# Performance work log

Hardware: AMD Instinct MI355X
Metric: run time of the kernel (lower is better)

Reference implementation:

```python
import jax, jax.numpy as jnp
import numpy as np

NUM_HEADS = 4
ALPHA = 0.2  # LeakyReLU negative slope


def setup_inputs() -> dict:
    key = jax.random.key(0)
    k1, k2 = jax.random.split(key)
    input_tensor = jax.random.normal(k1, (2, 4096, 128), dtype=jnp.float32)
    adj_matrix = jax.random.randint(k2, (4096, 4096), 0, 2, dtype=jnp.int32)
    return {"input_tensor": input_tensor, "adj_matrix": adj_matrix}


def reference(input_tensor, adj_matrix):
    B, S, F = input_tensor.shape
    H = NUM_HEADS
    x = input_tensor.reshape(B, S, H, F // H)          # (B,S,H,K)
    # full dense score matrix, QK^T-like with shared projection (identity)
    scores = jnp.einsum('bihk,bjhk->bhij', x, x)        # (B,H,S,S)
    scores = jax.nn.leaky_relu(scores, negative_slope=ALPHA)
    # adjacency mask broadcast over (B,H)
    scores = jnp.where(adj_matrix[None, None, :, :] == 0, -jnp.inf, scores)
    probs = jax.nn.softmax(scores, axis=-1)             # dropout p=0 -> identity
    out = jnp.einsum('bhij,bjhk->bihk', probs, x)       # (B,S,H,K)
    return out.reshape(B, S, F)                          # concat=True
```

## Files before the change

### kernel.cpp

```cpp
#include <hip/hip_runtime.h>
#include <stdint.h>

#define SEQ 4096
#define FDIM 128
#define NH 4
#define HD 32
#define NB 2
#define NROWS (NB * NH * SEQ)
#define LOG2E 1.4426950408889634f
#define VCOL 68
#define VHALF (32 * VCOL)

typedef float f32x4 __attribute__((ext_vector_type(4)));
typedef __bf16 bf16x8 __attribute__((ext_vector_type(8)));

__device__ __forceinline__ unsigned short f2bf(float f) {
  unsigned int u = __builtin_bit_cast(unsigned int, f);
  return (unsigned short)((u + 0x7FFFu + ((u >> 16) & 1u)) >> 16);
}

__global__ void cvt_kernel(const float* __restrict__ in, unsigned short* __restrict__ out) {
  int i = (blockIdx.x * 256 + threadIdx.x) * 4;
  float4 v = *reinterpret_cast<const float4*>(in + i);
  ushort4 o;
  o.x = f2bf(v.x); o.y = f2bf(v.y); o.z = f2bf(v.z); o.w = f2bf(v.w);
  *reinterpret_cast<ushort4*>(out + i) = o;
}

__global__ void adjpack_kernel(const int* __restrict__ adj, unsigned short* __restrict__ bits16) {
  size_t t = (size_t)blockIdx.x * 256 + threadIdx.x;
  const uint4* p = reinterpret_cast<const uint4*>(adj) + t * 4;
  uint4 a = p[0], b = p[1], c = p[2], d = p[3];
  unsigned m = 0;
  m |= (a.x != 0) ? 1u : 0u;        m |= (a.y != 0) ? 2u : 0u;
  m |= (a.z != 0) ? 4u : 0u;        m |= (a.w != 0) ? 8u : 0u;
  m |= (b.x != 0) ? 16u : 0u;       m |= (b.y != 0) ? 32u : 0u;
  m |= (b.z != 0) ? 64u : 0u;       m |= (b.w != 0) ? 128u : 0u;
  m |= (c.x != 0) ? 256u : 0u;      m |= (c.y != 0) ? 512u : 0u;
  m |= (c.z != 0) ? 1024u : 0u;     m |= (c.w != 0) ? 2048u : 0u;
  m |= (d.x != 0) ? 4096u : 0u;     m |= (d.y != 0) ? 8192u : 0u;
  m |= (d.z != 0) ? 16384u : 0u;    m |= (d.w != 0) ? 32768u : 0u;
  bits16[t] = (unsigned short)m;
}

#define STEP(T, RB, WBUF)                                                       \
  {                                                                             \
    __syncthreads();                                                            \
    const bool pfok = (T) + 1 < NT;                                             \
    if (pfok) {      \
      kptr += 64 * FDIM;                                                        \
      kload = *reinterpret_cast<const uint4*>(kptr);                            \
      sptr += 64 * FDIM;                                                        \
      r0 = *reinterpret_cast<const uint2*>(sptr);                               \
      r1 = *reinterpret_cast<const uint2*>(sptr + FDIM);                        \
      wnext = brow[bcol0 + (T) + 1];                                            \
    }                                                                           \
    f32x4 sc[4];                                                                \
    __builtin_amdgcn_s_setprio(1);                                              \
    _Pragma("unroll") for (int t4 = 0; t4 < 4; ++t4) {                          \
      bf16x8 kf = __builtin_bit_cast(bf16x8,                                    \
          *reinterpret_cast<const uint4*>(&Kl[RB][t4 * 16 + ql][g * 8]));       \
      sc[t4] = __builtin_amdgcn_mfma_f32_16x16x32_bf16(kf, qf, zf, 0, 0, 0);    \
    }                                                                           \
    __builtin_amdgcn_s_setprio(0);                                              \
    const unsigned long long wsh = wcur >> (4 * g);                             \
    const unsigned mwl = (unsigned)wsh, mwh = (unsigned)(wsh >> 32);            \
    float pf4[4][4];                                                            \
    _Pragma("unroll") for (int t4 = 0; t4 < 4; ++t4) {                          \
      const unsigned word = (t4 & 2) ? mwh : mwl;                               \
      _Pragma("unroll") for (int r = 0; r < 4; ++r) {                           \
        float v = sc[t4][r];                                                    \
        v = fmaxf(v, 0.2f * v);                                 \
        float e = __builtin_amdgcn_exp2f(v);                \
        const int pos = 16 * (t4 & 1) + r;                                      \
        const unsigned msk = (unsigned)((int)(word << (31 - pos)) >> 31);       \
        pf4[t4][r] = __builtin_bit_cast(                                        \
            float, __builtin_bit_cast(unsigned, e) & msk);                      \
      }                                                                         \
    }                                                                           \
    __builtin_amdgcn_s_setprio(1);                                              \
    _Pragma("unroll") for (int u = 0; u < 2; ++u) {                             \
      bf16x8 pa;                                                                \
      _Pragma("unroll") for (int tp = 0; tp < 2; ++tp)                          \
          _Pragma("unroll") for (int r = 0; r < 4; ++r)                         \
              pa[tp * 4 + r] = (__bf16)pf4[2 * u + tp][r];                      \
      bf16x8 vf0 = __builtin_bit_cast(bf16x8,                                   \
          *reinterpret_cast<const uint4*>(&Vp[RB][ql * VCOL + u * 32 + g * 8]));        \
      bf16x8 vf1 = __builtin_bit_cast(bf16x8,                                   \
          *reinterpret_cast<const uint4*>(&Vp[RB][(16 + ql) * VCOL + u * 32 + g * 8])); \
      acc0 = __builtin_amdgcn_mfma_f32_16x16x32_bf16(pa, vf0, acc0, 0, 0, 0);   \
      acc1 = __builtin_amdgcn_mfma_f32_16x16x32_bf16(pa, vf1, acc1, 0, 0, 0);   \
      accL = __builtin_amdgcn_mfma_f32_16x16x32_bf16(pa, ones, accL, 0, 0, 0);  \
    }                                                                           \
    __builtin_amdgcn_s_setprio(0);                                              \
    if (pfok) {   \
      *reinterpret_cast<uint4*>(&Kl[WBUF][krow][kq * 8]) = kload;               \
      unsigned* vw = reinterpret_cast<unsigned*>(&Vp[WBUF][0]) + pi0h;          \
      vw[(4 * c4 + 0) * 34] = __builtin_amdgcn_perm(r1.x, r0.x, selA);          \
      vw[(4 * c4 + 1) * 34] = __builtin_amdgcn_perm(r1.x, r0.x, selB);          \
      vw[(4 * c4 + 2) * 34] = __builtin_amdgcn_perm(r1.y, r0.y, selA);          \
      vw[(4 * c4 + 3) * 34] = __builtin_amdgcn_perm(r1.y, r0.y, selB);          \
    }                                                                           \
    wcur = wnext;                                                               \
  }

template <int NSPLIT>
__global__ __launch_bounds__(256, 4) void gat_kernel(
    const unsigned short* __restrict__ xbf,
    const unsigned long long* __restrict__ bits,
    float* __restrict__ dst,
    float* __restrict__ lbuf) {
  __shared__ __align__(16) unsigned short Kl[2][64][40];
  __shared__ __align__(16) unsigned short Vp[2][VHALF];

  const int bh = blockIdx.y;
  const int b = bh >> 2;
  const int h = bh & 3;
  const int tid = threadIdx.x;
  const int wid = tid >> 6;
  const int lane = tid & 63;
  const int g = lane >> 4;
  const int ql = lane & 15;
  const int qw = blockIdx.x * 64 + wid * 16;
  const int jbase = blockIdx.z * (SEQ / NSPLIT);
  const int NT = (SEQ / NSPLIT) / 64;

  const unsigned short* xb = xbf + ((size_t)b * SEQ) * FDIM + h * HD;

  bf16x8 qraw = __builtin_bit_cast(bf16x8,
      *reinterpret_cast<const uint4*>(xb + (size_t)(qw + ql) * FDIM + g * 8));
  bf16x8 qf;
#pragma unroll
  for (int e = 0; e < 8; ++e) qf[e] = (__bf16)((float)qraw[e] * LOG2E);

  bf16x8 ones;
#pragma unroll
  for (int e = 0; e < 8; ++e) ones[e] = (__bf16)1.0f;
  const f32x4 zf = {0.f, 0.f, 0.f, 0.f};

  f32x4 acc0 = {0.f, 0.f, 0.f, 0.f};
  f32x4 acc1 = {0.f, 0.f, 0.f, 0.f};
  f32x4 accL = {0.f, 0.f, 0.f, 0.f};

  const unsigned long long* brow = bits + (size_t)(qw + ql) * (SEQ / 64);
  const int bcol0 = jbase >> 6;

  const int krow = tid >> 2;
  const int kq = tid & 3;
  const unsigned short* kptr = xb + (size_t)(jbase + krow) * FDIM + kq * 8;

  const int s3 = (tid >> 3) & 7;
  const int pr = (s3 & 1) | (((s3 >> 1) & 1) << 1) | ((wid & 1) << 2) |
                 (((s3 >> 2) & 1) << 3) | ((wid >> 1) << 4);
  const int c4 = tid & 7;
  const unsigned short* sptr = xb + (size_t)(jbase + 2 * pr) * FDIM + c4 * 4;

  const int pi0h = 16 * (pr >> 4) + 4 * ((pr >> 1) & 3) + 2 * ((pr >> 3) & 1) + (pr & 1);

  const unsigned selA = 0x05040100u;
  const unsigned selB = 0x07060302u;

  uint4 kload = *reinterpret_cast<const uint4*>(kptr);
  uint2 r0 = *reinterpret_cast<const uint2*>(sptr);
  uint2 r1 = *reinterpret_cast<const uint2*>(sptr + FDIM);
  unsigned long long wcur = brow[bcol0];
  unsigned long long wnext = 0;
  *reinterpret_cast<uint4*>(&Kl[0][krow][kq * 8]) = kload;
  {
    unsigned* vw = reinterpret_cast<unsigned*>(&Vp[0][0]) + pi0h;
    vw[(4 * c4 + 0) * 34] = __builtin_amdgcn_perm(r1.x, r0.x, selA);
    vw[(4 * c4 + 1) * 34] = __builtin_amdgcn_perm(r1.x, r0.x, selB);
    vw[(4 * c4 + 2) * 34] = __builtin_amdgcn_perm(r1.y, r0.y, selA);
    vw[(4 * c4 + 3) * 34] = __builtin_amdgcn_perm(r1.y, r0.y, selB);
  }

  for (int t = 0; t < NT; t += 2) {
    STEP(t, 0, 1);
    STEP(t + 1, 1, 0);
  }

  if (NSPLIT == 1) {
#pragma unroll
    for (int r = 0; r < 4; ++r) {
      const float inv = 1.f / accL[r];
      const size_t o = ((size_t)b * SEQ + (size_t)(qw + 4 * g + r)) * FDIM + h * HD;
      dst[o + ql] = acc0[r] * inv;
      dst[o + 16 + ql] = acc1[r] * inv;
    }
  } else {
    float* Op = dst + (((size_t)blockIdx.z * (NB * NH) + bh) * SEQ) * HD;
#pragma unroll
    for (int r = 0; r < 4; ++r) {
      const int q = qw + 4 * g + r;
      Op[(size_t)q * HD + ql] = acc0[r];
      Op[(size_t)q * HD + 16 + ql] = acc1[r];
    }
    if (ql == 0) {
#pragma unroll
      for (int r = 0; r < 4; ++r)
        lbuf[(size_t)blockIdx.z * NROWS + (size_t)bh * SEQ + qw + 4 * g + r] = accL[r];
    }
  }
}

template <int NSPLIT>
__global__ __launch_bounds__(256) void combine_kernel(
    const float* __restrict__ Op, const float* __restrict__ lbuf, float* __restrict__ out) {
  const int idx = blockIdx.x * 256 + threadIdx.x;
  const int row = idx >> 3;
  const int dc = (idx & 7) * 4;
  float lt = 0.f;
  float4 o = {0.f, 0.f, 0.f, 0.f};
#pragma unroll
  for (int s = 0; s < NSPLIT; ++s) {
    lt += lbuf[(size_t)s * NROWS + row];
    float4 v = *reinterpret_cast<const float4*>(Op + ((size_t)s * NROWS + row) * HD + dc);
    o.x += v.x; o.y += v.y; o.z += v.z; o.w += v.w;
  }
  const float inv = 1.f / lt;
  const int bh = row >> 12;
  const int q = row & (SEQ - 1);
  const int b = bh >> 2;
  const int h = bh & 3;
  float4 w;
  w.x = o.x * inv; w.y = o.y * inv; w.z = o.z * inv; w.w = o.w * inv;
  *reinterpret_cast<float4*>(out + ((size_t)b * SEQ + q) * FDIM + h * HD + dc) = w;
}

extern "C" void kernel_launch(void* const* d_in, const int* in_sizes, int n_in,
                              void* d_out, int out_size, void* d_ws, size_t ws_size,
                              hipStream_t stream) {
  (void)in_sizes; (void)n_in; (void)out_size;
  const float* x = (const float*)d_in[0];
  const int* adj = (const int*)d_in[1];
  float* outp = (float*)d_out;

  unsigned short* xbf = (unsigned short*)d_ws;
  unsigned short* bits16 = (unsigned short*)((char*)d_ws + (2u << 20));
  float* Opart = (float*)((char*)d_ws + (4u << 20));
  auto need = [](int s) {
    return (size_t)(4u << 20) + (size_t)s * NROWS * HD * 4 + (size_t)s * NROWS * 4;
  };

  cvt_kernel<<<(NB * SEQ * FDIM) / (256 * 4), 256, 0, stream>>>(x, xbf);
  adjpack_kernel<<<(SEQ * SEQ) / (16 * 256), 256, 0, stream>>>(adj, bits16);

  const unsigned long long* bits = (const unsigned long long*)bits16;
  if (ws_size >= need(4)) {
    float* mlb = (float*)((char*)d_ws + (4u << 20) + (size_t)4 * NROWS * HD * 4);
    dim3 grid(SEQ / 64, NB * NH, 4);
    gat_kernel<4><<<grid, 256, 0, stream>>>(xbf, bits, Opart, mlb);
    combine_kernel<4><<<(NROWS * 8) / 256, 256, 0, stream>>>(Opart, mlb, outp);
  } else if (ws_size >= need(2)) {
    float* mlb = (float*)((char*)d_ws + (4u << 20) + (size_t)2 * NROWS * HD * 4);
    dim3 grid(SEQ / 64, NB * NH, 2);
    gat_kernel<2><<<grid, 256, 0, stream>>>(xbf, bits, Opart, mlb);
    combine_kernel<2><<<(NROWS * 8) / 256, 256, 0, stream>>>(Opart, mlb, outp);
  } else {
    dim3 grid(SEQ / 64, NB * NH, 1);
    gat_kernel<1><<<grid, 256, 0, stream>>>(xbf, bits, outp, nullptr);
  }
}
```

Before: 71.76 us.

## Double KV tile to 128 keys per barrier step and use sbfe mask extraction

Each pipeline step now processes 128 keys instead of 64, so the number of __syncthreads barriers and prefetch rounds is halved. K and V shared buffers, the V column stride and the adjacency bitmask loads (now a 128-bit load per step) are resized to match. Mask-bit extraction switches from a shift pair to a single signed bitfield extract. This doubles LDS use and raises register pressure, which could reduce occupancy under the launch bounds of 4 blocks.

```diff
diff --git a/kernel.cpp b/kernel.cpp
--- a/kernel.cpp
+++ b/kernel.cpp
@@ -8,8 +8,9 @@
 #define NB 2
 #define NROWS (NB * NH * SEQ)
 #define LOG2E 1.4426950408889634f
-#define VCOL 68
-#define VHALF (32 * VCOL)
+#define KVB 128
+#define VCS 136
+#define VPHALF (32 * VCS)
 
 typedef float f32x4 __attribute__((ext_vector_type(4)));
 typedef __bf16 bf16x8 __attribute__((ext_vector_type(8)));
@@ -48,60 +49,72 @@
     __syncthreads();                                                            \
     const bool pfok = (T) + 1 < NT;                                             \
     if (pfok) {      \
-      kptr += 64 * FDIM;                                                        \
-      kload = *reinterpret_cast<const uint4*>(kptr);                            \
-      sptr += 64 * FDIM;                                                        \
+      kptr += KVB * FDIM;                                                       \
+      k0 = *reinterpret_cast<const uint4*>(kptr);                               \
+      k1 = *reinterpret_cast<const uint4*>(kptr + 64 * FDIM);                   \
+      sptr += KVB * FDIM;                                                       \
       r0 = *reinterpret_cast<const uint2*>(sptr);                               \
       r1 = *reinterpret_cast<const uint2*>(sptr + FDIM);                        \
-      wnext = brow[bcol0 + (T) + 1];                                            \
+      r2 = *reinterpret_cast<const uint2*>(sptr + 64 * FDIM);                   \
+      r3 = *reinterpret_cast<const uint2*>(sptr + 65 * FDIM);                   \
+      wnv = *reinterpret_cast<const uint4*>(&brow[bcol0 + 2 * ((T) + 1)]);      \
     }                                                                           \
-    f32x4 sc[4];                                                                \
-    __builtin_amdgcn_s_setprio(1);                                              \
-    _Pragma("unroll") for (int t4 = 0; t4 < 4; ++t4) {                          \
-      bf16x8 kf = __builtin_bit_cast(bf16x8,                                    \
-          *reinterpret_cast<const uint4*>(&Kl[RB][t4 * 16 + ql][g * 8]));       \
-      sc[t4] = __builtin_amdgcn_mfma_f32_16x16x32_bf16(kf, qf, zf, 0, 0, 0);    \
+    _Pragma("unroll") for (int hf = 0; hf < 2; ++hf) {                          \
+      f32x4 sc[4];                                                              \
+      __builtin_amdgcn_s_setprio(1);                                            \
+      _Pragma("unroll") for (int t4 = 0; t4 < 4; ++t4) {                        \
+        bf16x8 kf = __builtin_bit_cast(bf16x8,                                  \
+            *reinterpret_cast<const uint4*>(                                    \
+                &Kl[RB][hf * 64 + t4 * 16 + ql][g * 8]));                       \
+        sc[t4] = __builtin_amdgcn_mfma_f32_16x16x32_bf16(kf, qf, zf, 0, 0, 0);  \
+      }                                                                         \
+      __builtin_amdgcn_s_setprio(0);                                            \
+      const unsigned long long wsh = (hf ? wc1 : wc0) >> (4 * g);               \
+      const int mwl = (int)(unsigned)wsh, mwh = (int)(unsigned)(wsh >> 32);     \
+      float pf4[4][4];                                                          \
+      _Pragma("unroll") for (int t4 = 0; t4 < 4; ++t4) {                        \
+        const int word = (t4 & 2) ? mwh : mwl;                                  \
+        _Pragma("unroll") for (int r = 0; r < 4; ++r) {                         \
+          float v = sc[t4][r];                                                  \
+          v = fmaxf(v, 0.2f * v);                               \
+          float e = __builtin_amdgcn_exp2f(v);              \
+          const int msk = __builtin_amdgcn_sbfe(word, 16 * (t4 & 1) + r, 1);    \
+          pf4[t4][r] = __builtin_bit_cast(                                      \
+              float, __builtin_bit_cast(unsigned, e) & (unsigned)msk);          \
+        }                                                                       \
+      }                                                                         \
+      __builtin_amdgcn_s_setprio(1);                                            \
+      _Pragma("unroll") for (int uu = 0; uu < 2; ++uu) {                        \
+        const int u = 2 * hf + uu;                                              \
+        bf16x8 pa;                                                              \
+        _Pragma("unroll") for (int tp = 0; tp < 2; ++tp)                        \
+            _Pragma("unroll") for (int r = 0; r < 4; ++r)                       \
+                pa[tp * 4 + r] = (__bf16)pf4[2 * uu + tp][r];                   \
+        bf16x8 vf0 = __builtin_bit_cast(bf16x8,                                 \
+            *reinterpret_cast<const uint4*>(&Vp[RB][ql * VCS + u * 32 + g * 8]));        \
+        bf16x8 vf1 = __builtin_bit_cast(bf16x8,                                 \
+            *reinterpret_cast<const uint4*>(&Vp[RB][(16 + ql) * VCS + u * 32 + g * 8])); \
+        acc0 = __builtin_amdgcn_mfma_f32_16x16x32_bf16(pa, vf0, acc0, 0, 0, 0); \
+        acc1 = __builtin_amdgcn_mfma_f32_16x16x32_bf16(pa, vf1, acc1, 0, 0, 0); \
+        accL = __builtin_amdgcn_mfma_f32_16x16x32_bf16(pa, ones, accL, 0, 0, 0);\
+      }                                                                         \
+      __builtin_amdgcn_s_setprio(0);                                            \
     }                                                                           \
-    __builtin_amdgcn_s_setprio(0);                                              \
-    const unsigned long long wsh = wcur >> (4 * g);                             \
-    const unsigned mwl = (unsigned)wsh, mwh = (unsigned)(wsh >> 32);            \
-    float pf4[4][4];                                                            \
-    _Pragma("unroll") for (int t4 = 0; t4 < 4; ++t4) {                          \
-      const unsigned word = (t4 & 2) ? mwh : mwl;                               \
-      _Pragma("unroll") for (int r = 0; r < 4; ++r) {                           \
-        float v = sc[t4][r];                                                    \
-        v = fmaxf(v, 0.2f * v);                                 \
-        float e = __builtin_amdgcn_exp2f(v);                \
-        const int pos = 16 * (t4 & 1) + r;                                      \
-        const unsigned msk = (unsigned)((int)(word << (31 - pos)) >> 31);       \
-        pf4[t4][r] = __builtin_bit_cast(                                        \
-            float, __builtin_bit_cast(unsigned, e) & msk);                      \
-      }                                                                         \
+    if (pfok) {   \
+      *reinterpret_cast<uint4*>(&Kl[WBUF][krow][kq * 8]) = k0;                  \
+      *reinterpret_cast<uint4*>(&Kl[WBUF][64 + krow][kq * 8]) = k1;             \
+      unsigned* vw = reinterpret_cast<unsigned*>(&Vp[WBUF][0]) + pi0h;          \
+      vw[(4 * c4 + 0) * 68] = __builtin_amdgcn_perm(r1.x, r0.x, selA);          \
+      vw[(4 * c4 + 1) * 68] = __builtin_amdgcn_perm(r1.x, r0.x, selB);          \
+      vw[(4 * c4 + 2) * 68] = __builtin_amdgcn_perm(r1.y, r0.y, selA);          \
+      vw[(4 * c4 + 3) * 68] = __builtin_amdgcn_perm(r1.y, r0.y, selB);          \
+      vw[(4 * c4 + 0) * 68 + 32] = __builtin_amdgcn_perm(r3.x, r2.x, selA);     \
+      vw[(4 * c4 + 1) * 68 + 32] = __builtin_amdgcn_perm(r3.x, r2.x, selB);     \
+      vw[(4 * c4 + 2) * 68 + 32] = __builtin_amdgcn_perm(r3.y, r2.y, selA);     \
+      vw[(4 * c4 + 3) * 68 + 32] = __builtin_amdgcn_perm(r3.y, r2.y, selB);     \
     }                                                                           \
-    __builtin_amdgcn_s_setprio(1);                                              \
-    _Pragma("unroll") for (int u = 0; u < 2; ++u) {                             \
-      bf16x8 pa;                                                                \
-      _Pragma("unroll") for (int tp = 0; tp < 2; ++tp)                          \
-          _Pragma("unroll") for (int r = 0; r < 4; ++r)                         \
-              pa[tp * 4 + r] = (__bf16)pf4[2 * u + tp][r];                      \
-      bf16x8 vf0 = __builtin_bit_cast(bf16x8,                                   \
-          *reinterpret_cast<const uint4*>(&Vp[RB][ql * VCOL + u * 32 + g * 8]));        \
-      bf16x8 vf1 = __builtin_bit_cast(bf16x8,                                   \
-          *reinterpret_cast<const uint4*>(&Vp[RB][(16 + ql) * VCOL + u * 32 + g * 8])); \
-      acc0 = __builtin_amdgcn_mfma_f32_16x16x32_bf16(pa, vf0, acc0, 0, 0, 0);   \
-      acc1 = __builtin_amdgcn_mfma_f32_16x16x32_bf16(pa, vf1, acc1, 0, 0, 0);   \
-      accL = __builtin_amdgcn_mfma_f32_16x16x32_bf16(pa, ones, accL, 0, 0, 0);  \
-    }                                                                           \
-    __builtin_amdgcn_s_setprio(0);                                              \
-    if (pfok) {   \
-      *reinterpret_cast<uint4*>(&Kl[WBUF][krow][kq * 8]) = kload;               \
-      unsigned* vw = reinterpret_cast<unsigned*>(&Vp[WBUF][0]) + pi0h;          \
-      vw[(4 * c4 + 0) * 34] = __builtin_amdgcn_perm(r1.x, r0.x, selA);          \
-      vw[(4 * c4 + 1) * 34] = __builtin_amdgcn_perm(r1.x, r0.x, selB);          \
-      vw[(4 * c4 + 2) * 34] = __builtin_amdgcn_perm(r1.y, r0.y, selA);          \
-      vw[(4 * c4 + 3) * 34] = __builtin_amdgcn_perm(r1.y, r0.y, selB);          \
-    }                                                                           \
-    wcur = wnext;                                                               \
+    wc0 = (unsigned long long)wnv.x | ((unsigned long long)wnv.y << 32);        \
+    wc1 = (unsigned long long)wnv.z | ((unsigned long long)wnv.w << 32);        \
   }
 
 template <int NSPLIT>
@@ -110,8 +123,8 @@
     const unsigned long long* __restrict__ bits,
     float* __restrict__ dst,
     float* __restrict__ lbuf) {
-  __shared__ __align__(16) unsigned short Kl[2][64][40];
-  __shared__ __align__(16) unsigned short Vp[2][VHALF];
+  __shared__ __align__(16) unsigned short Kl[2][KVB][40];
+  __shared__ __align__(16) unsigned short Vp[2][VPHALF];
 
   const int bh = blockIdx.y;
   const int b = bh >> 2;
@@ -123,7 +136,7 @@
   const int ql = lane & 15;
   const int qw = blockIdx.x * 64 + wid * 16;
   const int jbase = blockIdx.z * (SEQ / NSPLIT);
-  const int NT = (SEQ / NSPLIT) / 64;
+  const int NT = (SEQ / NSPLIT) / KVB;
 
   const unsigned short* xb = xbf + ((size_t)b * SEQ) * FDIM + h * HD;
 
@@ -160,18 +173,27 @@
   const unsigned selA = 0x05040100u;
   const unsigned selB = 0x07060302u;
 
-  uint4 kload = *reinterpret_cast<const uint4*>(kptr);
+  uint4 k0 = *reinterpret_cast<const uint4*>(kptr);
+  uint4 k1 = *reinterpret_cast<const uint4*>(kptr + 64 * FDIM);
   uint2 r0 = *reinterpret_cast<const uint2*>(sptr);
   uint2 r1 = *reinterpret_cast<const uint2*>(sptr + FDIM);
-  unsigned long long wcur = brow[bcol0];
-  unsigned long long wnext = 0;
-  *reinterpret_cast<uint4*>(&Kl[0][krow][kq * 8]) = kload;
+  uint2 r2 = *reinterpret_cast<const uint2*>(sptr + 64 * FDIM);
+  uint2 r3 = *reinterpret_cast<const uint2*>(sptr + 65 * FDIM);
+  uint4 wnv = *reinterpret_cast<const uint4*>(&brow[bcol0]);
+  unsigned long long wc0 = (unsigned long long)wnv.x | ((unsigned long long)wnv.y << 32);
+  unsigned long long wc1 = (unsigned long long)wnv.z | ((unsigned long long)wnv.w << 32);
+  *reinterpret_cast<uint4*>(&Kl[0][krow][kq * 8]) = k0;
+  *reinterpret_cast<uint4*>(&Kl[0][64 + krow][kq * 8]) = k1;
   {
     unsigned* vw = reinterpret_cast<unsigned*>(&Vp[0][0]) + pi0h;
-    vw[(4 * c4 + 0) * 34] = __builtin_amdgcn_perm(r1.x, r0.x, selA);
-    vw[(4 * c4 + 1) * 34] = __builtin_amdgcn_perm(r1.x, r0.x, selB);
-    vw[(4 * c4 + 2) * 34] = __builtin_amdgcn_perm(r1.y, r0.y, selA);
-    vw[(4 * c4 + 3) * 34] = __builtin_amdgcn_perm(r1.y, r0.y, selB);
+    vw[(4 * c4 + 0) * 68] = __builtin_amdgcn_perm(r1.x, r0.x, selA);
+    vw[(4 * c4 + 1) * 68] = __builtin_amdgcn_perm(r1.x, r0.x, selB);
+    vw[(4 * c4 + 2) * 68] = __builtin_amdgcn_perm(r1.y, r0.y, selA);
+    vw[(4 * c4 + 3) * 68] = __builtin_amdgcn_perm(r1.y, r0.y, selB);
+    vw[(4 * c4 + 0) * 68 + 32] = __builtin_amdgcn_perm(r3.x, r2.x, selA);
+    vw[(4 * c4 + 1) * 68 + 32] = __builtin_amdgcn_perm(r3.x, r2.x, selB);
+    vw[(4 * c4 + 2) * 68 + 32] = __builtin_amdgcn_perm(r3.y, r2.y, selA);
+    vw[(4 * c4 + 3) * 68 + 32] = __builtin_amdgcn_perm(r3.y, r2.y, selB);
   }
 
   for (int t = 0; t < NT; t += 2) {
```

Result: no change. 73.17 us (+2.0%).
